# Performance work log

Hardware: AMD Instinct MI355X
Metric: run time of the kernel (lower is better)

Reference implementation:

```python
import jax, jax.numpy as jnp
from jax import lax
import numpy as np

B, EMB, HEADS, LAYERS = 32, 512, 8, 4
SEQ_JD, TOK = 200, 50

def _mask_lg(S):
    # Faithful vectorization of CoKEModel.mask_lg (True = masked)
    m = np.ones((B, HEADS, S, S), dtype=bool)
    rows = np.arange(S)[:, None]
    cols = np.clip(rows - 5 + np.arange(10)[None, :], 0, S - 1)  # window=10, offset -5..4
    for h in range(6):  # local_len = 6 local-window heads
        m[:, h, rows, cols] = False
    m[0, 6:] = False          # global heads unmasked only for batch 0 (faithful to source)
    m[:, :, 0, :] = False     # CLS row attends everywhere
    return m

def _ln_free(x):
    # CoKEModel.layer_norm: no affine, eps=1e-12, rsqrt form
    mu = jnp.mean(x, axis=-1, keepdims=True)
    sx = x - mu
    v = jnp.mean(sx * sx, axis=-1, keepdims=True)
    return sx * jnp.sqrt(1.0 / (v + 1e-12))

def _ln(x, g, b):
    mu = jnp.mean(x, axis=-1, keepdims=True)
    sx = x - mu
    v = jnp.mean(sx * sx, axis=-1, keepdims=True)
    return sx / jnp.sqrt(v + 1e-5) * g + b

def _textcnn(tokens, emb, cws, cbs, fw, fb):
    e = emb[tokens]                        # (N, 50, 1024)
    x = jnp.transpose(e, (0, 2, 1))        # (N, 1024, 50): embed dim as channels
    pooled = []
    for W, b in zip(cws, cbs):             # W: (100, k, 1024)
        rhs = jnp.transpose(W, (0, 2, 1))  # (100, 1024, k)
        y = lax.conv_general_dilated(x, rhs, (1,), 'VALID', dimension_numbers=('NCH', 'OIH', 'NCH'))
        y = jax.nn.relu(y + b[None, :, None])
        pooled.append(jnp.max(y, axis=2))  # global max-pool over time
    return jnp.concatenate(pooled, axis=1) @ fw.T + fb   # (N, 512)

def _encoder(x, mask, wq, bq, wk, bk, wv, bv, wo, bo, l1g, l1b, fw1, fb1, fw2, fb2, l2g, l2b):
    Bb, S, D = x.shape
    dh = D // HEADS
    scale = 1.0 / (dh ** 0.5)
    for l in range(LAYERS):
        q = (x @ wq[l].T + bq[l]).reshape(Bb, S, HEADS, dh)
        k = (x @ wk[l].T + bk[l]).reshape(Bb, S, HEADS, dh)
        v = (x @ wv[l].T + bv[l]).reshape(Bb, S, HEADS, dh)
        s = jnp.einsum('bshd,bthd->bhst', q, k) * scale
        s = jnp.where(mask, -1e9, s)
        a = jax.nn.softmax(s, axis=-1)
        c = jnp.einsum('bhst,bthd->bshd', a, v).reshape(Bb, S, D)
        x = _ln(x + c @ wo[l].T + bo[l], l1g[l], l1b[l])
        h = jax.nn.relu(x @ fw1[l].T + fb1[l])
        x = _ln(x + h @ fw2[l].T + fb2[l], l2g[l], l2b[l])
    return x

def _contrastive(im, s, margin=0.02):
    sc = im @ s.T
    d = jnp.diag(sc)
    cs = jnp.maximum(margin + sc - d[:, None], 0.0)
    ci = jnp.maximum(margin + sc - d[None, :], 0.0)
    eye = jnp.eye(sc.shape[0], dtype=bool)
    cs = jnp.where(eye, 0.0, cs)
    ci = jnp.where(eye, 0.0, ci)
    return jnp.sum(cs) + jnp.sum(ci)

def _forward(floats, src, mask101, mask200):
    (user_info, label_similarity, emb_tc, cw1, cb1, cw2, cb2, cw3, cb3, tfw, tfb,
     wq, bq, wk, bk, wv, bv, wo, bo, l1g, l1b, fw1, fb1, fw2, fb2, l2g, l2b,
     fc1w, fc1b, fc2w, fc2b, fc3w, fc3b, fc4w, fc4b, pscale, pbias) = floats
    cws, cbs = (cw1, cw2, cw3), (cb1, cb2, cb3)
    enc = (wq, bq, wk, bk, wv, bv, wo, bo, l1g, l1b, fw1, fb1, fw2, fb2, l2g, l2b)

    # ---- first pass: first 100 JDs + global CLS token ----
    s1 = _textcnn(src[:, :100].reshape(-1, TOK), emb_tc, cws, cbs, tfw, tfb).reshape(B, 100, EMB)
    s1 = _ln_free(s1)
    s1 = jnp.concatenate([jnp.zeros((B, 1, EMB), s1.dtype), s1], axis=1)  # (B, 101, EMB)
    p = _encoder(s1, mask101, *enc)
    p = jax.nn.gelu(p @ fc1w.T + fc1b, approximate=False)
    p = _ln_free(p)
    p = p * pscale[:, :p.shape[1]] + pbias[:, :p.shape[1]]
    p = p @ fc2w.T + fc2b                      # (B, 101, 204)
    cls_e, tok = p[:, :1], p[:, 1:]
    P = tok @ fc3w.T + fc3b                    # (B, 100, 204)
    clsIII = cls_e @ fc3w.T + fc3b             # (B, 1, 204)
    SLl = jnp.einsum('bsm,bsn->bmn', P, P)     # P^T @ P
    SL_hat = label_similarity[None] + 0.4 * SLl
    outIII = jnp.squeeze(clsIII @ SL_hat, axis=1)  # (B, 204)

    # ---- second pass: all 200 JDs ----
    s2 = _textcnn(src.reshape(-1, TOK), emb_tc, cws, cbs, tfw, tfb).reshape(B, SEQ_JD, EMB)
    s2 = _ln_free(s2)
    ap = _encoder(s2, mask200, *enc)
    ap = jax.nn.gelu(ap @ fc1w.T + fc1b, approximate=False)
    ap = _ln_free(ap)
    ap = ap * pscale[:, :SEQ_JD] + pbias[:, :SEQ_JD]
    p1 = ap @ fc2w.T + fc2b                    # (B, 200, 204)

    nn_ = SEQ_JD // 100  # = 2 neighbors
    eps = 1e-6
    skl_rows, seuc_rows = [], []
    for i in range(nn_):
        # NOTE: faithful to source slicing bug: [i : (i+1)*100]
        c1 = jax.nn.softmax(jnp.mean(p1[:, i:(i + 1) * 100], axis=1), axis=-1)
        a1 = jax.nn.softmax(jnp.mean(ap[:, i:(i + 1) * 100], axis=1), axis=-1)
        rk, re = [], []
        for j in range(nn_):
            c2 = jax.nn.softmax(jnp.mean(p1[:, j:(j + 1) * 100], axis=1), axis=-1)
            a2 = jax.nn.softmax(jnp.mean(ap[:, j:(j + 1) * 100], axis=1), axis=-1)
            rk.append(jnp.sum((c1 + eps) * jnp.log((c1 + eps) / (c2 + eps)), axis=-1))
            re.append(jnp.sqrt(jnp.sum((a1 - a2) ** 2, axis=-1) + 1e-12))
        skl_rows.append(jnp.stack(rk, axis=-1))
        seuc_rows.append(jnp.stack(re, axis=-1))
    skl = jnp.stack(skl_rows, axis=1).reshape(B, -1) * 10.0
    seuc = jnp.stack(seuc_rows, axis=1).reshape(B, -1)
    skl = jax.nn.softmax(skl, axis=-1)
    seuc = jax.nn.softmax(seuc, axis=-1)
    loss_sims = jnp.mean(jnp.sum((skl + eps) * jnp.log((skl + eps) / (seuc + eps)), axis=-1))

    cls4m = jnp.squeeze(cls_e, axis=1)
    user4m = user_info @ fc4w.T + fc4b
    nrm = lambda x: x / jnp.maximum(jnp.linalg.norm(x, axis=1, keepdims=True), 1e-12)
    match = _contrastive(nrm(cls4m), nrm(user4m))

    return (jax.nn.softmax(outIII, axis=-1),
            jax.nn.softmax(cls_e, axis=-1),
            loss_sims * 100000.0,
            match * 0.01)

def setup_inputs():
    key = jax.random.key(0)
    kit = iter(jax.random.split(key, 48))
    def nrm(shape, s=0.02):
        return jax.random.normal(next(kit), shape, jnp.float32) * s
    d = {}
    d['src'] = jax.random.randint(next(kit), (B, SEQ_JD, TOK), 0, 20000)
    d['user_info'] = nrm((B, 142), 1.0)
    d['label_similarity'] = nrm((204, 204))
    d['emb_tc'] = nrm((20000, 1024)).at[0].set(0.0)  # padding_idx=0 row zeroed
    d['cw1'], d['cb1'] = nrm((100, 1, 1024)), jnp.zeros((100,), jnp.float32)
    d['cw2'], d['cb2'] = nrm((100, 2, 1024)), jnp.zeros((100,), jnp.float32)
    d['cw3'], d['cb3'] = nrm((100, 3, 1024)), jnp.zeros((100,), jnp.float32)
    d['tfw'], d['tfb'] = nrm((512, 300)), jnp.zeros((512,), jnp.float32)
    d['wq'], d['bq'] = nrm((LAYERS, EMB, EMB)), jnp.zeros((LAYERS, EMB), jnp.float32)
    d['wk'], d['bk'] = nrm((LAYERS, EMB, EMB)), jnp.zeros((LAYERS, EMB), jnp.float32)
    d['wv'], d['bv'] = nrm((LAYERS, EMB, EMB)), jnp.zeros((LAYERS, EMB), jnp.float32)
    d['wo'], d['bo'] = nrm((LAYERS, EMB, EMB)), jnp.zeros((LAYERS, EMB), jnp.float32)
    d['l1g'], d['l1b'] = jnp.ones((LAYERS, EMB), jnp.float32), jnp.zeros((LAYERS, EMB), jnp.float32)
    d['fw1'], d['fb1'] = nrm((LAYERS, 2048, EMB)), jnp.zeros((LAYERS, 2048), jnp.float32)
    d['fw2'], d['fb2'] = nrm((LAYERS, EMB, 2048)), jnp.zeros((LAYERS, EMB), jnp.float32)
    d['l2g'], d['l2b'] = jnp.ones((LAYERS, EMB), jnp.float32), jnp.zeros((LAYERS, EMB), jnp.float32)
    d['fc1w'], d['fc1b'] = nrm((EMB, EMB)), jnp.zeros((EMB,), jnp.float32)
    d['fc2w'], d['fc2b'] = nrm((204, EMB)), jnp.zeros((204,), jnp.float32)
    d['fc3w'], d['fc3b'] = nrm((204, 204)), jnp.zeros((204,), jnp.float32)
    d['fc4w'], d['fc4b'] = nrm((204, 142)), jnp.zeros((204,), jnp.float32)
    d['pscale'] = jnp.ones((B, 300, EMB), jnp.float32)
    d['pbias'] = jnp.zeros((B, 300, EMB), jnp.float32)
    d['mask101'] = jnp.asarray(_mask_lg(101))
    d['mask200'] = jnp.asarray(_mask_lg(SEQ_JD))
    return d

def reference(src, user_info, label_similarity, emb_tc, cw1, cb1, cw2, cb2, cw3, cb3, tfw, tfb, wq, bq, wk, bk, wv, bv, wo, bo, l1g, l1b, fw1, fb1, fw2, fb2, l2g, l2b, fc1w, fc1b, fc2w, fc2b, fc3w, fc3b, fc4w, fc4b, pscale, pbias, mask101, mask200):
    floats = (user_info, label_similarity, emb_tc, cw1, cb1, cw2, cb2, cw3, cb3, tfw, tfb,
              wq, bq, wk, bk, wv, bv, wo, bo, l1g, l1b, fw1, fb1, fw2, fb2, l2g, l2b,
              fc1w, fc1b, fc2w, fc2b, fc3w, fc3b, fc4w, fc4b, pscale, pbias)
    return _forward(floats, src, mask101, mask200)
```

## Files before the change

kernel.cpp:

```cpp
#include <hip/hip_runtime.h>
#include <math.h>

#define EMB 512
#define HEADS 8
#define NLAYERS 4
#define NB 32
#define SEQ 200
#define TOKN 50
#define DH 64
#define FFND 2048
#define NCLS 204
#define VC 640
#define KD 1024
#define CCH 8
#define CROWS (6400/CCH)
#define CM (CROWS*TOKN)
#define MSEG 16

typedef __attribute__((ext_vector_type(8))) short v8s;
typedef __attribute__((ext_vector_type(4))) float v4f;
typedef unsigned short ushort_t;

__device__ __forceinline__ ushort_t f2bu(float f){
  unsigned u = __float_as_uint(f);
  return (ushort_t)((u + 0x7FFFu + ((u >> 16) & 1u)) >> 16);
}
__device__ __forceinline__ float bu2f(ushort_t u){
  return __uint_as_float(((unsigned)u) << 16);
}

__device__ __forceinline__ float block_reduce(float v, float* red, int nwaves, bool domax){
  int tid = threadIdx.x;
  #pragma unroll
  for (int o = 32; o > 0; o >>= 1){
    float t = __shfl_down(v, o, 64);
    v = domax ? fmaxf(v, t) : (v + t);
  }
  __syncthreads();
  if ((tid & 63) == 0) red[tid >> 6] = v;
  __syncthreads();
  float r = red[0];
  for (int i = 1; i < nwaves; i++) r = domax ? fmaxf(r, red[i]) : (r + red[i]);
  return r;
}

__global__ void prep_w_kernel(const float* __restrict__ cw1, const float* __restrict__ cw2,
                              const float* __restrict__ cw3, ushort_t* __restrict__ Wb){
  int idx4 = blockIdx.x * 256 + threadIdx.x;
  if (idx4 >= VC * KD / 4) return;
  int row = idx4 >> 8;
  int k = (idx4 & 255) * 4;
  float4 v = make_float4(0.f, 0.f, 0.f, 0.f);
  const float* s = nullptr;
  if (row < 100)      s = cw1 + (size_t)row * KD;
  else if (row < 200) s = cw2 + (size_t)((row - 100) * 2 + 0) * KD;
  else if (row < 300) s = cw2 + (size_t)((row - 200) * 2 + 1) * KD;
  else if (row < 400) s = cw3 + (size_t)((row - 300) * 3 + 0) * KD;
  else if (row < 500) s = cw3 + (size_t)((row - 400) * 3 + 1) * KD;
  else if (row < 600) s = cw3 + (size_t)((row - 500) * 3 + 2) * KD;
  if (s) v = *(const float4*)(s + k);
  ushort4 o;
  o.x = f2bu(v.x); o.y = f2bu(v.y); o.z = f2bu(v.z); o.w = f2bu(v.w);
  *(ushort4*)(Wb + (size_t)row * KD + k) = o;
}

__global__ void prep_tfwT_kernel(const float* __restrict__ tfw, float* __restrict__ tfwT){
  int idx = blockIdx.x * 256 + threadIdx.x;
  if (idx >= 300 * EMB) return;
  int j = idx >> 9, o = idx & 511;
  tfwT[(size_t)j * EMB + o] = tfw[(size_t)o * 300 + j];
}

__global__ void split_kernel(const float* __restrict__ src, ushort_t* __restrict__ hi,
                             ushort_t* __restrict__ lo, int n){
  int i4 = (blockIdx.x * 256 + threadIdx.x) * 4;
  if (i4 >= n) return;
  float4 f = *(const float4*)(src + i4);
  float x[4] = {f.x, f.y, f.z, f.w};
  ushort4 h, l;
  ushort_t hh[4], ll[4];
  #pragma unroll
  for (int e = 0; e < 4; e++){
    unsigned u = __float_as_uint(x[e]);
    float hf = __uint_as_float(u & 0xFFFF0000u);
    hh[e] = (ushort_t)(u >> 16);
    ll[e] = f2bu(x[e] - hf);
  }
  h.x=hh[0]; h.y=hh[1]; h.z=hh[2]; h.w=hh[3];
  l.x=ll[0]; l.y=ll[1]; l.z=ll[2]; l.w=ll[3];
  *(ushort4*)(hi + i4) = h;
  *(ushort4*)(lo + i4) = l;
}

__global__ void qkvbias_kernel(const float* __restrict__ bq, const float* __restrict__ bk,
                               const float* __restrict__ bv, float* __restrict__ bqkv){
  int l = blockIdx.x;
  for (int j = threadIdx.x; j < 1536; j += 256){
    float v;
    if (j < 512) v = bq[l * 512 + j];
    else if (j < 1024) v = bk[l * 512 + j - 512];
    else v = bv[l * 512 + j - 1024];
    bqkv[l * 1536 + j] = v;
  }
}

__global__ __launch_bounds__(256, 4) void conv_gemm_kernel(
    const int* __restrict__ tok, const float* __restrict__ emb,
    const ushort_t* __restrict__ Wb, ushort_t* __restrict__ Cout, int Mc)
{
  __shared__ ushort_t Al[128][40];
  __shared__ ushort_t Bl[128][40];
  const int tid = threadIdx.x;
  const int n0 = blockIdx.x * 128;
  const int m0 = blockIdx.y * 128;
  const int wave = tid >> 6, lane = tid & 63;
  const int wm = (wave >> 1) * 64, wn = (wave & 1) * 64;
  const int lcol = lane & 15, lq = lane >> 4;

  v4f acc[4][4];
  #pragma unroll
  for (int i = 0; i < 4; i++)
    #pragma unroll
    for (int j = 0; j < 4; j++) acc[i][j] = (v4f){0.f, 0.f, 0.f, 0.f};

  const int srow = tid >> 1, skh = (tid & 1) * 16;
  const int am = m0 + srow;
  const float* aep = (am < Mc) ? (emb + (size_t)tok[am] * KD + skh) : nullptr;
  const ushort_t* bep = Wb + (size_t)(n0 + srow) * KD + skh;

  for (int k0 = 0; k0 < KD; k0 += 32){
    uint4 p0 = make_uint4(0,0,0,0), p1 = make_uint4(0,0,0,0);
    if (aep){
      float4 f0 = *(const float4*)(aep + k0);
      float4 f1 = *(const float4*)(aep + k0 + 4);
      float4 f2 = *(const float4*)(aep + k0 + 8);
      float4 f3 = *(const float4*)(aep + k0 + 12);
      p0.x = (unsigned)f2bu(f0.x) | ((unsigned)f2bu(f0.y) << 16);
      p0.y = (unsigned)f2bu(f0.z) | ((unsigned)f2bu(f0.w) << 16);
      p0.z = (unsigned)f2bu(f1.x) | ((unsigned)f2bu(f1.y) << 16);
      p0.w = (unsigned)f2bu(f1.z) | ((unsigned)f2bu(f1.w) << 16);
      p1.x = (unsigned)f2bu(f2.x) | ((unsigned)f2bu(f2.y) << 16);
      p1.y = (unsigned)f2bu(f2.z) | ((unsigned)f2bu(f2.w) << 16);
      p1.z = (unsigned)f2bu(f3.x) | ((unsigned)f2bu(f3.y) << 16);
      p1.w = (unsigned)f2bu(f3.z) | ((unsigned)f2bu(f3.w) << 16);
    }
    *(uint4*)&Al[srow][skh]     = p0;
    *(uint4*)&Al[srow][skh + 8] = p1;
    uint4 b0 = *(const uint4*)(bep + k0);
    uint4 b1 = *(const uint4*)(bep + k0 + 8);
    *(uint4*)&Bl[srow][skh]     = b0;
    *(uint4*)&Bl[srow][skh + 8] = b1;
    __syncthreads();

    v8s af[4];
    #pragma unroll
    for (int mi = 0; mi < 4; mi++)
      af[mi] = *(const v8s*)&Al[wm + mi*16 + lcol][lq*8];
    #pragma unroll
    for (int ni = 0; ni < 4; ni++){
      v8s bf = *(const v8s*)&Bl[wn + ni*16 + lcol][lq*8];
      #pragma unroll
      for (int mi = 0; mi < 4; mi++)
        acc[mi][ni] = __builtin_amdgcn_mfma_f32_16x16x32_bf16(af[mi], bf, acc[mi][ni], 0, 0, 0);
    }
    __syncthreads();
  }

  #pragma unroll
  for (int ni = 0; ni < 4; ni++){
    int n = n0 + wn + ni*16 + lcol;
    #pragma unroll
    for (int mi = 0; mi < 4; mi++){
      int mbase = m0 + wm + mi*16 + lq*4;
      #pragma unroll
      for (int rg = 0; rg < 4; rg++){
        int m = mbase + rg;
        if (m < Mc) Cout[(size_t)m * VC + n] = f2bu(acc[mi][ni][rg]);
      }
    }
  }
}

__global__ __launch_bounds__(256, 2) void pool_fc_kernel(
    const ushort_t* __restrict__ Cc, const float* __restrict__ tfwT,
    const float* __restrict__ cb1, const float* __restrict__ cb2,
    const float* __restrict__ cb3, const float* __restrict__ tfb,
    float* __restrict__ basep)
{
  __shared__ ushort_t Sg[VC][54];
  __shared__ float pooled[304];
  __shared__ float red[8];
  const int tid = threadIdx.x;
  const int r = blockIdx.x;

  const unsigned* cr = (const unsigned*)(Cc + (size_t)r * TOKN * VC);
  for (int p = 0; p < TOKN; p++){
    for (int t = tid; t < VC/2; t += 256){
      unsigned u = cr[p * (VC/2) + t];
      Sg[2*t][p]   = (ushort_t)(u & 0xFFFFu);
      Sg[2*t+1][p] = (ushort_t)(u >> 16);
    }
  }
  __syncthreads();

  for (int c = tid; c < 300; c += 256){
    float mv = -1e30f;
    if (c < 100){
      float bb = cb1[c];
      for (int p = 0; p < 50; p++) mv = fmaxf(mv, bu2f(Sg[c][p]) + bb);
    } else if (c < 200){
      int o = c - 100; float bb = cb2[o];
      for (int p = 0; p < 49; p++)
        mv = fmaxf(mv, bu2f(Sg[100 + o][p]) + bu2f(Sg[200 + o][p + 1]) + bb);
    } else {
      int o = c - 200; float bb = cb3[o];
      for (int p = 0; p < 48; p++)
        mv = fmaxf(mv, bu2f(Sg[300 + o][p]) + bu2f(Sg[400 + o][p + 1]) + bu2f(Sg[500 + o][p + 2]) + bb);
    }
    pooled[c] = fmaxf(mv, 0.f);
  }
  __syncthreads();

  float v0 = tfb[tid], v1 = tfb[tid + 256];
  for (int j = 0; j < 300; j++){
    float pj = pooled[j];
    v0 = fmaf(pj, tfwT[(size_t)j * EMB + tid], v0);
    v1 = fmaf(pj, tfwT[(size_t)j * EMB + tid + 256], v1);
  }
  float tot = block_reduce(v0 + v1, red, 4, false);
  float mu = tot * (1.f / 512.f);
  float s0 = v0 - mu, s1 = v1 - mu;
  float var = block_reduce(s0 * s0 + s1 * s1, red, 4, false) * (1.f / 512.f);
  float sc = sqrtf(1.f / (var + 1e-12f));
  basep[(size_t)r * EMB + tid] = s0 * sc;
  basep[(size_t)r * EMB + tid + 256] = s1 * sc;
}

__global__ __launch_bounds__(256, 3) void gemm_mfma_pre_kernel(
    const float* __restrict__ A, const ushort_t* __restrict__ Whi,
    const ushort_t* __restrict__ Wlo, const float* __restrict__ bias,
    float* __restrict__ C, int M, int N, int K, int ldc, int act)
{
  __shared__ ushort_t Ahi[128][40];
  __shared__ ushort_t Alo[128][40];
  __shared__ ushort_t Bhi[128][40];
  __shared__ ushort_t Blo[128][40];

  const int tid = threadIdx.x;
  const int m0 = blockIdx.y * 128, n0 = blockIdx.x * 128;
  const int wave = tid >> 6, lane = tid & 63;
  const int wm = (wave >> 1) * 64, wn = (wave & 1) * 64;
  const int lcol = lane & 15, lq = lane >> 4;

  v4f acc[4][4];
  #pragma unroll
  for (int i = 0; i < 4; i++)
    #pragma unroll
    for (int j = 0; j < 4; j++) acc[i][j] = (v4f){0.f, 0.f, 0.f, 0.f};

  const int srow = tid >> 1;
  const int skh  = (tid & 1) * 16;
  const int am = m0 + srow, bn = n0 + srow;
  const bool mok = (am < M), nok = (bn < N);
  const float* ap = A + (size_t)am * K + skh;
  const ushort_t* bph = Whi + (size_t)bn * K + skh;
  const ushort_t* bpl = Wlo + (size_t)bn * K + skh;

  for (int k0 = 0; k0 < K; k0 += 32){
    bool kfull = (k0 + 32 <= K);
    {
      float av[16];
      if (mok && kfull){
        #pragma unroll
        for (int q = 0; q < 4; q++){
          float4 f = *(const float4*)(ap + k0 + q*4);
          av[q*4+0]=f.x; av[q*4+1]=f.y; av[q*4+2]=f.z; av[q*4+3]=f.w;
        }
      } else {
        #pragma unroll
        for (int e = 0; e < 16; e++){
          int k = k0 + skh + e;
          av[e] = (mok && k < K) ? ap[k0 + e] : 0.f;
        }
      }
      uint4 uh[2], ul[2];
      #pragma unroll
      for (int h = 0; h < 2; h++){
        unsigned hw[8], lw[8];
        #pragma unroll
        for (int e = 0; e < 8; e++){
          float x = av[h*8+e];
          unsigned u = __float_as_uint(x);
          float hf = __uint_as_float(u & 0xFFFF0000u);
          hw[e] = u >> 16;
          lw[e] = f2bu(x - hf);
        }
        uh[h] = make_uint4(hw[0]|(hw[1]<<16), hw[2]|(hw[3]<<16), hw[4]|(hw[5]<<16), hw[6]|(hw[7]<<16));
        ul[h] = make_uint4(lw[0]|(lw[1]<<16), lw[2]|(lw[3]<<16), lw[4]|(lw[5]<<16), lw[6]|(lw[7]<<16));
      }
      *(uint4*)&Ahi[srow][skh]     = uh[0];
      *(uint4*)&Ahi[srow][skh + 8] = uh[1];
      *(uint4*)&Alo[srow][skh]     = ul[0];
      *(uint4*)&Alo[srow][skh + 8] = ul[1];
    }
    {
      uint4 h0 = make_uint4(0,0,0,0), h1 = h0, l0 = h0, l1 = h0;
      if (nok && kfull){
        h0 = *(const uint4*)(bph + k0);
        h1 = *(const uint4*)(bph + k0 + 8);
        l0 = *(const uint4*)(bpl + k0);
        l1 = *(const uint4*)(bpl + k0 + 8);
      } else if (nok){
        ushort_t he[16], le[16];
        #pragma unroll
        for (int e = 0; e < 16; e++){
          int k = k0 + skh + e;
          he[e] = (k < K) ? bph[k0 + e] : (ushort_t)0;
          le[e] = (k < K) ? bpl[k0 + e] : (ushort_t)0;
        }
        h0 = *(uint4*)&he[0]; h1 = *(uint4*)&he[8];
        l0 = *(uint4*)&le[0]; l1 = *(uint4*)&le[8];
      }
      *(uint4*)&Bhi[srow][skh]     = h0;
      *(uint4*)&Bhi[srow][skh + 8] = h1;
      *(uint4*)&Blo[srow][skh]     = l0;
      *(uint4*)&Blo[srow][skh + 8] = l1;
    }
    __syncthreads();

    v8s ah[4], al[4];
    #pragma unroll
    for (int mi = 0; mi < 4; mi++){
      ah[mi] = *(const v8s*)&Ahi[wm + mi*16 + lcol][lq*8];
      al[mi] = *(const v8s*)&Alo[wm + mi*16 + lcol][lq*8];
    }
    #pragma unroll
    for (int ni = 0; ni < 4; ni++){
      v8s bh = *(const v8s*)&Bhi[wn + ni*16 + lcol][lq*8];
      v8s bl = *(const v8s*)&Blo[wn + ni*16 + lcol][lq*8];
      #pragma unroll
      for (int mi = 0; mi < 4; mi++){
        acc[mi][ni] = __builtin_amdgcn_mfma_f32_16x16x32_bf16(ah[mi], bh, acc[mi][ni], 0, 0, 0);
        acc[mi][ni] = __builtin_amdgcn_mfma_f32_16x16x32_bf16(al[mi], bh, acc[mi][ni], 0, 0, 0);
        acc[mi][ni] = __builtin_amdgcn_mfma_f32_16x16x32_bf16(ah[mi], bl, acc[mi][ni], 0, 0, 0);
      }
    }
    __syncthreads();
  }

  #pragma unroll
  for (int ni = 0; ni < 4; ni++){
    int n = n0 + wn + ni*16 + lcol;
    if (n >= N) continue;
    float bv = bias[n];
    #pragma unroll
    for (int mi = 0; mi < 4; mi++){
      int mbase = m0 + wm + mi*16 + lq*4;
      #pragma unroll
      for (int rg = 0; rg < 4; rg++){
        int m = mbase + rg;
        if (m >= M) continue;
        float v = acc[mi][ni][rg] + bv;
        if (act == 1) v = fmaxf(v, 0.f);
        else if (act == 2) v = 0.5f * v * (1.f + erff(v * 0.70710678118654752f));
        C[(size_t)m * ldc + n] = v;
      }
    }
  }
}

__global__ __launch_bounds__(256, 2) void gemm_mfma_kernel(
    const float* __restrict__ A, const float* __restrict__ W,
    const float* __restrict__ bias, float* __restrict__ C,
    int M, int N, int K, int ldc, int act)
{
  __shared__ ushort_t Ahi[128][40];
  __shared__ ushort_t Alo[128][40];
  __shared__ ushort_t Bhi[128][40];
  __shared__ ushort_t Blo[128][40];

  const int tid = threadIdx.x;
  const int m0 = blockIdx.y * 128, n0 = blockIdx.x * 128;
  const int wave = tid >> 6, lane = tid & 63;
  const int wm = (wave >> 1) * 64, wn = (wave & 1) * 64;
  const int lcol = lane & 15, lq = lane >> 4;

  v4f acc[4][4];
  #pragma unroll
  for (int i = 0; i < 4; i++)
    #pragma unroll
    for (int j = 0; j < 4; j++) acc[i][j] = (v4f){0.f, 0.f, 0.f, 0.f};

  const int srow = tid >> 1;
  const int skh  = (tid & 1) * 16;

  for (int k0 = 0; k0 < K; k0 += 32){
    {
      float av[16];
      int m = m0 + srow;
      const float* ap = A + (size_t)m * K + k0 + skh;
      bool mok = (m < M);
      if (mok && (k0 + 32 <= K)){
        #pragma unroll
        for (int q = 0; q < 4; q++){
          float4 f = ((const float4*)ap)[q];
          av[q*4+0]=f.x; av[q*4+1]=f.y; av[q*4+2]=f.z; av[q*4+3]=f.w;
        }
      } else {
        #pragma unroll
        for (int e = 0; e < 16; e++){
          int k = k0 + skh + e;
          av[e] = (mok && k < K) ? ap[e] : 0.f;
        }
      }
      uint4 uh[2], ul[2];
      #pragma unroll
      for (int h = 0; h < 2; h++){
        unsigned hw[8], lw[8];
        #pragma unroll
        for (int e = 0; e < 8; e++){
          float x = av[h*8+e];
          unsigned u = __float_as_uint(x);
          float hf = __uint_as_float(u & 0xFFFF0000u);
          hw[e] = u >> 16;
          lw[e] = f2bu(x - hf);
        }
        uh[h] = make_uint4(hw[0]|(hw[1]<<16), hw[2]|(hw[3]<<16), hw[4]|(hw[5]<<16), hw[6]|(hw[7]<<16));
        ul[h] = make_uint4(lw[0]|(lw[1]<<16), lw[2]|(lw[3]<<16), lw[4]|(lw[5]<<16), lw[6]|(lw[7]<<16));
      }
      *(uint4*)&Ahi[srow][skh]     = uh[0];
      *(uint4*)&Ahi[srow][skh + 8] = uh[1];
      *(uint4*)&Alo[srow][skh]     = ul[0];
      *(uint4*)&Alo[srow][skh + 8] = ul[1];
    }
    {
      float bv[16];
      int n = n0 + srow;
      const float* bp = W + (size_t)n * K + k0 + skh;
      bool nok = (n < N);
      if (nok && (k0 + 32 <= K)){
        #pragma unroll
        for (int q = 0; q < 4; q++){
          float4 f = ((const float4*)bp)[q];
          bv[q*4+0]=f.x; bv[q*4+1]=f.y; bv[q*4+2]=f.z; bv[q*4+3]=f.w;
        }
      } else {
        #pragma unroll
        for (int e = 0; e < 16; e++){
          int k = k0 + skh + e;
          bv[e] = (nok && k < K) ? bp[e] : 0.f;
        }
      }
      uint4 uh[2], ul[2];
      #pragma unroll
      for (int h = 0; h < 2; h++){
        unsigned hw[8], lw[8];
        #pragma unroll
        for (int e = 0; e < 8; e++){
          float x = bv[h*8+e];
          unsigned u = __float_as_uint(x);
          float hf = __uint_as_float(u & 0xFFFF0000u);
          hw[e] = u >> 16;
          lw[e] = f2bu(x - hf);
        }
        uh[h] = make_uint4(hw[0]|(hw[1]<<16), hw[2]|(hw[3]<<16), hw[4]|(hw[5]<<16), hw[6]|(hw[7]<<16));
        ul[h] = make_uint4(lw[0]|(lw[1]<<16), lw[2]|(lw[3]<<16), lw[4]|(lw[5]<<16), lw[6]|(lw[7]<<16));
      }
      *(uint4*)&Bhi[srow][skh]     = uh[0];
      *(uint4*)&Bhi[srow][skh + 8] = uh[1];
      *(uint4*)&Blo[srow][skh]     = ul[0];
      *(uint4*)&Blo[srow][skh + 8] = ul[1];
    }
    __syncthreads();

    v8s ah[4], al[4];
    #pragma unroll
    for (int mi = 0; mi < 4; mi++){
      ah[mi] = *(const v8s*)&Ahi[wm + mi*16 + lcol][lq*8];
      al[mi] = *(const v8s*)&Alo[wm + mi*16 + lcol][lq*8];
    }
    #pragma unroll
    for (int ni = 0; ni < 4; ni++){
      v8s bh = *(const v8s*)&Bhi[wn + ni*16 + lcol][lq*8];
      v8s bl = *(const v8s*)&Blo[wn + ni*16 + lcol][lq*8];
      #pragma unroll
      for (int mi = 0; mi < 4; mi++){
        acc[mi][ni] = __builtin_amdgcn_mfma_f32_16x16x32_bf16(ah[mi], bh, acc[mi][ni], 0, 0, 0);
        acc[mi][ni] = __builtin_amdgcn_mfma_f32_16x16x32_bf16(al[mi], bh, acc[mi][ni], 0, 0, 0);
        acc[mi][ni] = __builtin_amdgcn_mfma_f32_16x16x32_bf16(ah[mi], bl, acc[mi][ni], 0, 0, 0);
      }
    }
    __syncthreads();
  }

  #pragma unroll
  for (int ni = 0; ni < 4; ni++){
    int n = n0 + wn + ni*16 + lcol;
    if (n >= N) continue;
    float bv = bias[n];
    #pragma unroll
    for (int mi = 0; mi < 4; mi++){
      int mbase = m0 + wm + mi*16 + lq*4;
      #pragma unroll
      for (int rg = 0; rg < 4; rg++){
        int m = mbase + rg;
        if (m >= M) continue;
        float v = acc[mi][ni][rg] + bv;
        if (act == 1) v = fmaxf(v, 0.f);
        else if (act == 2) v = 0.5f * v * (1.f + erff(v * 0.70710678118654752f));
        C[(size_t)m * ldc + n] = v;
      }
    }
  }
}

__global__ __launch_bounds__(256) void gemm_kernel(
    const float* __restrict__ A, const float* __restrict__ W,
    const float* __restrict__ bias, float* __restrict__ C,
    int M, int N, int K, int act)
{
  __shared__ float As[16][64];
  __shared__ float Ws[16][64];
  const int tid = threadIdx.x;
  const int m0 = blockIdx.y * 64, n0 = blockIdx.x * 64;
  const int lr = tid >> 2;
  const int lk = (tid & 3) * 4;
  const int tx = tid & 15, ty = tid >> 4;
  float cc[4][4];
  #pragma unroll
  for (int i = 0; i < 4; i++)
    #pragma unroll
    for (int j = 0; j < 4; j++) cc[i][j] = 0.f;

  for (int k0 = 0; k0 < K; k0 += 16){
    #pragma unroll
    for (int i = 0; i < 4; i++){
      int k = k0 + lk + i;
      int m = m0 + lr;
      As[lk + i][lr] = (m < M && k < K) ? A[(size_t)m * K + k] : 0.f;
      int n = n0 + lr;
      Ws[lk + i][lr] = (n < N && k < K) ? W[(size_t)n * K + k] : 0.f;
    }
    __syncthreads();
    #pragma unroll
    for (int kk = 0; kk < 16; kk++){
      float4 a = *(const float4*)&As[kk][ty * 4];
      float4 b = *(const float4*)&Ws[kk][tx * 4];
      float av[4] = {a.x, a.y, a.z, a.w};
      float bv[4] = {b.x, b.y, b.z, b.w};
      #pragma unroll
      for (int i = 0; i < 4; i++)
        #pragma unroll
        for (int j = 0; j < 4; j++) cc[i][j] = fmaf(av[i], bv[j], cc[i][j]);
    }
    __syncthreads();
  }

  #pragma unroll
  for (int i = 0; i < 4; i++){
    int m = m0 + ty * 4 + i;
    if (m >= M) continue;
    #pragma unroll
    for (int j = 0; j < 4; j++){
      int n = n0 + tx * 4 + j;
      if (n >= N) continue;
      float v = cc[i][j] + bias[n];
      if (act == 1) v = fmaxf(v, 0.f);
      else if (act == 2) v = 0.5f * v * (1.f + erff(v * 0.70710678118654752f));
      C[(size_t)m * N + n] = v;
    }
  }
}

__global__ __launch_bounds__(256) void ln_kernel(
    const float* __restrict__ X, const float* __restrict__ Res,
    const float* __restrict__ g, const float* __restrict__ bta,
    const float* __restrict__ pscale, const float* __restrict__ pbias,
    float* __restrict__ Y, int S, float eps)
{
  __shared__ float red[8];
  const int r = blockIdx.x, tid = threadIdx.x;
  size_t o0 = (size_t)r * EMB + tid;
  size_t o1 = o0 + 256;
  float v0 = X[o0] + (Res ? Res[o0] : 0.f);
  float v1 = X[o1] + (Res ? Res[o1] : 0.f);
  float tot = block_reduce(v0 + v1, red, 4, false);
  float mu = tot * (1.f / 512.f);
  float s0 = v0 - mu, s1 = v1 - mu;
  float var = block_reduce(s0 * s0 + s1 * s1, red, 4, false) * (1.f / 512.f);
  float rs = 1.f / sqrtf(var + eps);
  float y0 = s0 * rs, y1 = s1 * rs;
  if (g){
    y0 = y0 * g[tid] + bta[tid];
    y1 = y1 * g[tid + 256] + bta[tid + 256];
  }
  if (pscale){
    int b = r / S, t = r % S;
    size_t po = ((size_t)(b * 300 + t)) * EMB;
    y0 = y0 * pscale[po + tid] + pbias[po + tid];
    y1 = y1 * pscale[po + tid + 256] + pbias[po + tid + 256];
  }
  Y[o0] = y0;
  Y[o1] = y1;
}

__global__ __launch_bounds__(64) void vmean_kernel(const float* __restrict__ qkv,
                                                   float* __restrict__ vm, int S){
  int bh = blockIdx.x; int b = bh >> 3, h = bh & 7; int d = threadIdx.x;
  const float* vr = qkv + (size_t)(b * S) * 1536 + 1024 + h * DH + d;
  float s = 0.f;
  for (int j = 0; j < S; j++) s += vr[(size_t)j * 1536];
  vm[bh * DH + d] = s / (float)S;
}

__global__ __launch_bounds__(64) void attn_kernel(
    const float* __restrict__ qkv, const float* __restrict__ vm,
    float* __restrict__ Ctx, int S)
{
  __shared__ float qv[DH];
  __shared__ float sc[SEQ];
  __shared__ float wts[16];
  const int tid = threadIdx.x;
  const int blk = blockIdx.x;
  const int i = blk % S;
  const int bh = blk / S;
  const int h = bh % HEADS;
  const int b = bh / HEADS;
  const size_t rowoff = ((size_t)(b * S + i)) * 1536 + h * DH;
  const size_t coff = ((size_t)(b * S + i)) * EMB + h * DH;
  const bool rowall = (i == 0) || (b == 0 && h >= 6);

  if (rowall){
    qv[tid] = qkv[rowoff + tid];
    __syncthreads();
    for (int j = tid; j < S; j += 64){
      const float* kr = qkv + ((size_t)(b * S + j)) * 1536 + 512 + h * DH;
      float d = 0.f;
      #pragma unroll
      for (int d4 = 0; d4 < 16; d4++){
        float4 kk = *(const float4*)(kr + d4 * 4);
        d = fmaf(qv[d4*4+0], kk.x, d);
        d = fmaf(qv[d4*4+1], kk.y, d);
        d = fmaf(qv[d4*4+2], kk.z, d);
        d = fmaf(qv[d4*4+3], kk.w, d);
      }
      sc[j] = d * 0.125f;
    }
    __syncthreads();
    float mx = -INFINITY;
    for (int j = tid; j < S; j += 64) mx = fmaxf(mx, sc[j]);
    #pragma unroll
    for (int o = 32; o > 0; o >>= 1) mx = fmaxf(mx, __shfl_down(mx, o, 64));
    mx = __shfl(mx, 0, 64);
    float sm = 0.f;
    for (int j = tid; j < S; j += 64){ float e = expf(sc[j] - mx); sc[j] = e; sm += e; }
    #pragma unroll
    for (int o = 32; o > 0; o >>= 1) sm += __shfl_down(sm, o, 64);
    sm = __shfl(sm, 0, 64);
    float inv = 1.f / sm;
    __syncthreads();
    float a_ = 0.f;
    const float* vr = qkv + ((size_t)(b * S)) * 1536 + 1024 + h * DH + tid;
    for (int j = 0; j < S; j++) a_ = fmaf(sc[j], vr[(size_t)j * 1536], a_);
    Ctx[coff + tid] = a_ * inv;
  } else if (h < 6){
    qv[tid] = qkv[rowoff + tid];
    __syncthreads();
    const int lo = max(0, i - 5), hi = min(S - 1, i + 4);
    const int cnt = hi - lo + 1;
    float s = -INFINITY;
    if (tid < cnt){
      const float* kr = qkv + ((size_t)(b * S + lo + tid)) * 1536 + 512 + h * DH;
      float d = 0.f;
      #pragma unroll
      for (int d4 = 0; d4 < 16; d4++){
        float4 kk = *(const float4*)(kr + d4 * 4);
        d = fmaf(qv[d4*4+0], kk.x, d);
        d = fmaf(qv[d4*4+1], kk.y, d);
        d = fmaf(qv[d4*4+2], kk.z, d);
        d = fmaf(qv[d4*4+3], kk.w, d);
      }
      s = d * 0.125f;
    }
    float mx = s;
    #pragma unroll
    for (int o = 8; o > 0; o >>= 1) mx = fmaxf(mx, __shfl_xor(mx, o, 16));
    float e = (tid < cnt) ? expf(s - mx) : 0.f;
    float sm = e;
    #pragma unroll
    for (int o = 8; o > 0; o >>= 1) sm += __shfl_xor(sm, o, 16);
    if (tid < 16) wts[tid] = e / sm;
    __syncthreads();
    float a_ = 0.f;
    const float* vr = qkv + ((size_t)(b * S + lo)) * 1536 + 1024 + h * DH + tid;
    for (int j = 0; j < cnt; j++) a_ = fmaf(wts[j], vr[(size_t)j * 1536], a_);
    Ctx[coff + tid] = a_;
  } else {
    Ctx[coff + tid] = vm[(b * HEADS + h) * DH + tid];
  }
}

__global__ void buildx1_kernel(const float* __restrict__ base, float* __restrict__ x1){
  int idx = blockIdx.x * 256 + threadIdx.x;
  if (idx >= NB * 101 * EMB) return;
  int e = idx & 511;
  int bt = idx >> 9;
  int t = bt % 101, b = bt / 101;
  x1[idx] = (t == 0) ? 0.f : base[((size_t)(b * SEQ + t - 1)) * EMB + e];
}

__global__ void extract_kernel(const float* __restrict__ p2, float* __restrict__ clsE, float* __restrict__ tok){
  int idx = blockIdx.x * 256 + threadIdx.x;
  if (idx >= NB * 101 * NCLS) return;
  int n = idx % NCLS;
  int bt = idx / NCLS;
  int t = bt % 101, b = bt / 101;
  float v = p2[idx];
  if (t == 0) clsE[b * NCLS + n] = v;
  else tok[((size_t)(b * 100 + t - 1)) * NCLS + n] = v;
}

__global__ void zero_kernel(float* p){ if (threadIdx.x == 0) p[0] = 0.f; }

__global__ __launch_bounds__(256) void slhat_kernel(
    const float* __restrict__ P, const float* __restrict__ ls, float* __restrict__ SLh)
{
  int bm = blockIdx.x;
  int b = bm / NCLS, m = bm % NCLS;
  int n = threadIdx.x;
  if (n >= NCLS) return;
  const float* Pb = P + (size_t)b * 100 * NCLS;
  float s = 0.f;
  for (int t = 0; t < 100; t++) s = fmaf(Pb[t * NCLS + m], Pb[t * NCLS + n], s);
  SLh[((size_t)bm) * NCLS + n] = ls[m * NCLS + n] + 0.4f * s;
}

__global__ __launch_bounds__(256) void outIII_kernel(
    const float* __restrict__ cls3, const float* __restrict__ SLh, float* __restrict__ o3)
{
  int b = blockIdx.x, n = threadIdx.x;
  if (n >= NCLS) return;
  float s = 0.f;
  for (int m = 0; m < NCLS; m++)
    s = fmaf(cls3[b * NCLS + m], SLh[((size_t)(b * NCLS + m)) * NCLS + n], s);
  o3[b * NCLS + n] = s;
}

__global__ __launch_bounds__(256) void softmax_out_kernel(const float* __restrict__ X, float* __restrict__ O, int n){
  __shared__ float red[8];
  int r = blockIdx.x, tid = threadIdx.x;
  float mx = -INFINITY;
  for (int j = tid; j < n; j += 256) mx = fmaxf(mx, X[(size_t)r * n + j]);
  mx = block_reduce(mx, red, 4, true);
  float sm = 0.f;
  for (int j = tid; j < n; j += 256) sm += expf(X[(size_t)r * n + j] - mx);
  sm = block_reduce(sm, red, 4, false);
  for (int j = tid; j < n; j += 256) O[(size_t)r * n + j] = expf(X[(size_t)r * n + j] - mx) / sm;
}

__global__ __launch_bounds__(256) void normalize_kernel(
    const float* __restrict__ clsE, const float* __restrict__ u4,
    float* __restrict__ imn, float* __restrict__ sn)
{
  __shared__ float red[8];
  int r = blockIdx.x, tid = threadIdx.x;
  const float* s = (r < NB) ? (clsE + (size_t)r * NCLS) : (u4 + (size_t)(r - NB) * NCLS);
  float* d = (r < NB) ? (imn + (size_t)r * NCLS) : (sn + (size_t)(r - NB) * NCLS);
  float v = (tid < NCLS) ? s[tid] : 0.f;
  float ss = block_reduce(v * v, red, 4, false);
  float nrm = fmaxf(sqrtf(ss), 1e-12f);
  if (tid < NCLS) d[tid] = v / nrm;
}

__global__ __launch_bounds__(1024) void contrastive_kernel(
    const float* __restrict__ imn, const float* __restrict__ sn, float* __restrict__ out)
{
  __shared__ float sc[NB][NB];
  __shared__ float red[16];
  int tid = threadIdx.x;
  int i = tid >> 5, j = tid & 31;
  float d = 0.f;
  for (int c = 0; c < NCLS; c++) d = fmaf(imn[i * NCLS + c], sn[j * NCLS + c], d);
  sc[i][j] = d;
  __syncthreads();
  float di = sc[i][i], dj = sc[j][j];
  float v = 0.f;
  if (i != j)
    v = fmaxf(0.02f + sc[i][j] - di, 0.f) + fmaxf(0.02f + sc[i][j] - dj, 0.f);
  #pragma unroll
  for (int o = 32; o > 0; o >>= 1) v += __shfl_down(v, o, 64);
  if ((tid & 63) == 0) red[tid >> 6] = v;
  __syncthreads();
  if (tid == 0){
    float s = 0.f;
    for (int w = 0; w < 16; w++) s += red[w];
    out[13057] = s * 0.01f;
  }
}

__global__ __launch_bounds__(256) void means_part_kernel(
    const float* __restrict__ p1, const float* __restrict__ ap,
    float* __restrict__ part)
{
  const int blk = blockIdx.x;
  const int bi = blk / MSEG, seg = blk % MSEG;
  const int b = bi >> 1, i = bi & 1;
  const int start = i;
  const int cnt = (i == 0) ? 100 : 199;
  const int per = (cnt + MSEG - 1) / MSEG;
  const int r0 = seg * per;
  const int r1 = min(r0 + per, cnt);
  float* dst = part + (size_t)blk * 720;
  for (int c = threadIdx.x; c < NCLS + EMB; c += 256){
    float s = 0.f;
    if (c < NCLS){
      for (int rr = r0; rr < r1; rr++)
        s += p1[((size_t)(b * SEQ + start + rr)) * NCLS + c];
    } else {
      int cc = c - NCLS;
      for (int rr = r0; rr < r1; rr++)
        s += ap[((size_t)(b * SEQ + start + rr)) * EMB + cc];
    }
    dst[c] = s;
  }
}

__global__ __launch_bounds__(256) void means_final_kernel(
    const float* __restrict__ part, float* __restrict__ mp, float* __restrict__ ma)
{
  const int bi = blockIdx.x;
  const int i = bi & 1;
  const float icnt = (i == 0) ? (1.f / 100.f) : (1.f / 199.f);
  for (int c = threadIdx.x; c < NCLS + EMB; c += 256){
    float s = 0.f;
    #pragma unroll
    for (int g = 0; g < MSEG; g++)
      s += part[((size_t)(bi * MSEG + g)) * 720 + c];
    if (c < NCLS) mp[(size_t)bi * NCLS + c] = s * icnt;
    else          ma[(size_t)bi * EMB + (c - NCLS)] = s * icnt;
  }
}

__global__ __launch_bounds__(64) void klfinal_kernel(
    const float* __restrict__ cbuf, const float* __restrict__ abuf, float* __restrict__ acc)
{
  const int b = blockIdx.x, lane = threadIdx.x;
  float rk[4], re[4];
  #pragma unroll
  for (int pr = 0; pr < 4; pr++){
    int i = pr >> 1, j = pr & 1;
    const float* c1 = cbuf + ((size_t)(b * 2 + i)) * NCLS;
    const float* c2 = cbuf + ((size_t)(b * 2 + j)) * NCLS;
    float s = 0.f;
    for (int n = lane; n < NCLS; n += 64){
      float x = c1[n] + 1e-6f, y = c2[n] + 1e-6f;
      s += x * logf(x / y);
    }
    #pragma unroll
    for (int o = 32; o > 0; o >>= 1) s += __shfl_down(s, o, 64);
    rk[pr] = __shfl(s, 0, 64);
    const float* a1 = abuf + ((size_t)(b * 2 + i)) * EMB;
    const float* a2 = abuf + ((size_t)(b * 2 + j)) * EMB;
    float s2 = 0.f;
    for (int n = lane; n < EMB; n += 64){
      float dd = a1[n] - a2[n];
      s2 += dd * dd;
    }
    #pragma unroll
    for (int o = 32; o > 0; o >>= 1) s2 += __shfl_down(s2, o, 64);
    re[pr] = sqrtf(__shfl(s2, 0, 64) + 1e-12f);
  }
  if (lane == 0){
    float sk[4], se[4];
    float mk = -INFINITY, me = -INFINITY;
    for (int p = 0; p < 4; p++){
      sk[p] = rk[p] * 10.f;
      mk = fmaxf(mk, sk[p]);
      se[p] = re[p];
      me = fmaxf(me, se[p]);
    }
    float ssk = 0.f, sse = 0.f;
    for (int p = 0; p < 4; p++){ sk[p] = expf(sk[p] - mk); ssk += sk[p]; se[p] = expf(se[p] - me); sse += se[p]; }
    float loss = 0.f;
    for (int p = 0; p < 4; p++){
      float x = sk[p] / ssk + 1e-6f, y = se[p] / sse + 1e-6f;
      loss += x * logf(x / y);
    }
    atomicAdd(acc, loss);
  }
}

__global__ void finalize_kernel(const float* __restrict__ acc, float* __restrict__ out){
  if (threadIdx.x == 0) out[13056] = acc[0] * (100000.f / 32.f);
}

extern "C" void kernel_launch(void* const* d_in, const int* in_sizes, int n_in,
                              void* d_out, int out_size, void* d_ws, size_t ws_size,
                              hipStream_t stream)
{
  (void)in_sizes; (void)n_in; (void)out_size;
  const int*   src  = (const int*)  d_in[0];
  const float* user_info = (const float*)d_in[1];
  const float* ls   = (const float*)d_in[2];
  const float* emb  = (const float*)d_in[3];
  const float* cw1  = (const float*)d_in[4];  const float* cb1 = (const float*)d_in[5];
  const float* cw2  = (const float*)d_in[6];  const float* cb2 = (const float*)d_in[7];
  const float* cw3  = (const float*)d_in[8];  const float* cb3 = (const float*)d_in[9];
  const float* tfw  = (const float*)d_in[10]; const float* tfb = (const float*)d_in[11];
  const float* wq   = (const float*)d_in[12]; const float* bq  = (const float*)d_in[13];
  const float* wk   = (const float*)d_in[14]; const float* bk  = (const float*)d_in[15];
  const float* wv   = (const float*)d_in[16]; const float* bv  = (const float*)d_in[17];
  const float* wo   = (const float*)d_in[18]; const float* bo  = (const float*)d_in[19];
  const float* l1g  = (const float*)d_in[20]; const float* l1b = (const float*)d_in[21];
  const float* fw1  = (const float*)d_in[22]; const float* fb1 = (const float*)d_in[23];
  const float* fw2  = (const float*)d_in[24]; const float* fb2 = (const float*)d_in[25];
  const float* l2g  = (const float*)d_in[26]; const float* l2b = (const float*)d_in[27];
  const float* fc1w = (const float*)d_in[28]; const float* fc1b= (const float*)d_in[29];
  const float* fc2w = (const float*)d_in[30]; const float* fc2b= (const float*)d_in[31];
  const float* fc3w = (const float*)d_in[32]; const float* fc3b= (const float*)d_in[33];
  const float* fc4w = (const float*)d_in[34]; const float* fc4b= (const float*)d_in[35];
  const float* pscale = (const float*)d_in[36];
  const float* pbias  = (const float*)d_in[37];
  float* out = (float*)d_out;
  float* ws = (float*)d_ws;

  size_t off = 0;
  auto alloc = [&](size_t n){ float* p = ws + off; off += ((n + 3) & ~(size_t)3); return p; };
  float* base = alloc(6400ULL * EMB);
  float* x1   = alloc((size_t)NB * 101 * EMB);
  float* qkv  = alloc(6400ULL * 1536);
  float* ctx  = alloc(6400ULL * EMB);
  float* proj = alloc(6400ULL * EMB);
  float* hb   = alloc(6400ULL * FFND);
  float* p2   = alloc(6400ULL * NCLS);
  float* clsE = alloc((size_t)NB * NCLS);
  float* tok  = alloc(3200ULL * NCLS);
  float* Pb   = alloc(3200ULL * NCLS);
  float* cls3 = alloc((size_t)NB * NCLS);
  float* SLh  = alloc((size_t)NB * NCLS * NCLS);
  float* o3   = alloc((size_t)NB * NCLS);
  float* u4   = alloc((size_t)NB * NCLS);
  float* imn  = alloc((size_t)NB * NCLS);
  float* sn   = alloc((size_t)NB * NCLS);
  float* mp   = alloc(64ULL * NCLS);
  float* ma   = alloc(64ULL * EMB);
  float* cbf  = alloc(64ULL * NCLS);
  float* abf  = alloc(64ULL * EMB);
  float* lacc = alloc(4);
  float* vmb  = alloc((size_t)NB * HEADS * DH);
  ushort_t* Wb = (ushort_t*)alloc((size_t)VC * KD / 2);
  float* tfwT = alloc(300ULL * EMB);
  float* bqkv = alloc(4ULL * 1536);
  const size_t OQKV = 0, OWO = 3145728, OF1 = 4194304, OF2 = 8388608;
  const size_t OC1 = 12582912, OC2 = 12845056, OC3 = 12949504, WTOT = 12991120;
  ushort_t* WhiA = (ushort_t*)alloc((WTOT + 1) / 2);
  ushort_t* WloA = (ushort_t*)alloc((WTOT + 1) / 2);
  const bool presplit = (off * sizeof(float) <= ws_size);

  auto gemm_f32 = [&](const float* A, const float* W, const float* bi, float* C,
                      int M, int N, int K, int act){
    dim3 g((N + 63) / 64, (M + 63) / 64);
    gemm_kernel<<<g, 256, 0, stream>>>(A, W, bi, C, M, N, K, act);
  };
  auto gemm_fly = [&](const float* A, const float* W, const float* bi, float* C,
                      int M, int N, int K, int ldc, int act){
    dim3 g((N + 127) / 128, (M + 127) / 128);
    gemm_mfma_kernel<<<g, 256, 0, stream>>>(A, W, bi, C, M, N, K, ldc, act);
  };
  auto gemm_pre = [&](const float* A, size_t woff, const float* bi, float* C,
                      int M, int N, int K, int ldc, int act){
    dim3 g((N + 127) / 128, (M + 127) / 128);
    gemm_mfma_pre_kernel<<<g, 256, 0, stream>>>(A, WhiA + woff, WloA + woff, bi, C, M, N, K, ldc, act);
  };
  auto split = [&](const float* srcw, size_t woff, int n){
    split_kernel<<<(n / 4 + 255) / 256, 256, 0, stream>>>(srcw, WhiA + woff, WloA + woff, n);
  };

  prep_w_kernel<<<(VC * KD / 4 + 255) / 256, 256, 0, stream>>>(cw1, cw2, cw3, Wb);
  prep_tfwT_kernel<<<(300 * EMB + 255) / 256, 256, 0, stream>>>(tfw, tfwT);
  if (presplit){
    for (int l = 0; l < NLAYERS; l++){
      split(wq + (size_t)l * 262144, OQKV + (size_t)l * 786432,          262144);
      split(wk + (size_t)l * 262144, OQKV + (size_t)l * 786432 + 262144, 262144);
      split(wv + (size_t)l * 262144, OQKV + (size_t)l * 786432 + 524288, 262144);
      split(wo + (size_t)l * 262144, OWO + (size_t)l * 262144, 262144);
      split(fw1 + (size_t)l * 1048576, OF1 + (size_t)l * 1048576, 1048576);
      split(fw2 + (size_t)l * 1048576, OF2 + (size_t)l * 1048576, 1048576);
    }
    split(fc1w, OC1, 262144);
    split(fc2w, OC2, NCLS * EMB);
    split(fc3w, OC3, NCLS * NCLS);
    qkvbias_kernel<<<4, 256, 0, stream>>>(bq, bk, bv, bqkv);
  }

  for (int c = 0; c < CCH; c++){
    conv_gemm_kernel<<<dim3(VC / 128, (CM + 127) / 128), 256, 0, stream>>>(
        src + (size_t)c * CM, emb, Wb, (ushort_t*)hb, CM);
    pool_fc_kernel<<<CROWS, 256, 0, stream>>>(
        (ushort_t*)hb, tfwT, cb1, cb2, cb3, tfb, base + (size_t)c * CROWS * EMB);
  }
  buildx1_kernel<<<(NB * 101 * EMB + 255) / 256, 256, 0, stream>>>(base, x1);

  auto encoder = [&](float* x, int S){
    int M = NB * S;
    for (int l = 0; l < NLAYERS; l++){
      if (presplit){
        gemm_pre(x, OQKV + (size_t)l * 786432, bqkv + l * 1536, qkv, M, 1536, EMB, 1536, 0);
      } else {
        gemm_fly(x, wq + (size_t)l * EMB * EMB, bq + l * EMB, qkv,        M, EMB, EMB, 1536, 0);
        gemm_fly(x, wk + (size_t)l * EMB * EMB, bk + l * EMB, qkv + 512,  M, EMB, EMB, 1536, 0);
        gemm_fly(x, wv + (size_t)l * EMB * EMB, bv + l * EMB, qkv + 1024, M, EMB, EMB, 1536, 0);
      }
      vmean_kernel<<<NB * HEADS, 64, 0, stream>>>(qkv, vmb, S);
      attn_kernel<<<NB * HEADS * S, 64, 0, stream>>>(qkv, vmb, ctx, S);
      if (presplit) gemm_pre(ctx, OWO + (size_t)l * 262144, bo + l * EMB, proj, M, EMB, EMB, EMB, 0);
      else gemm_fly(ctx, wo + (size_t)l * EMB * EMB, bo + l * EMB, proj, M, EMB, EMB, EMB, 0);
      ln_kernel<<<M, 256, 0, stream>>>(proj, x, l1g + l * EMB, l1b + l * EMB, nullptr, nullptr, x, S, 1e-5f);
      if (presplit) gemm_pre(x, OF1 + (size_t)l * 1048576, fb1 + l * FFND, hb, M, FFND, EMB, FFND, 1);
      else gemm_fly(x, fw1 + (size_t)l * FFND * EMB, fb1 + l * FFND, hb, M, FFND, EMB, FFND, 1);
      if (presplit) gemm_pre(hb, OF2 + (size_t)l * 1048576, fb2 + l * EMB, proj, M, EMB, FFND, EMB, 0);
      else gemm_fly(hb, fw2 + (size_t)l * EMB * FFND, fb2 + l * EMB, proj, M, EMB, FFND, EMB, 0);
      ln_kernel<<<M, 256, 0, stream>>>(proj, x, l2g + l * EMB, l2b + l * EMB, nullptr, nullptr, x, S, 1e-5f);
    }
    if (presplit) gemm_pre(x, OC1, fc1b, ctx, M, EMB, EMB, EMB, 2);
    else gemm_fly(x, fc1w, fc1b, ctx, M, EMB, EMB, EMB, 2);
    ln_kernel<<<M, 256, 0, stream>>>(ctx, nullptr, nullptr, nullptr, pscale, pbias, ctx, S, 1e-12f);
    if (presplit) gemm_pre(ctx, OC2, fc2b, p2, M, NCLS, EMB, NCLS, 0);
    else gemm_fly(ctx, fc2w, fc2b, p2, M, NCLS, EMB, NCLS, 0);
  };

  encoder(x1, 101);
  extract_kernel<<<(NB * 101 * NCLS + 255) / 256, 256, 0, stream>>>(p2, clsE, tok);
  if (presplit) gemm_pre(tok, OC3, fc3b, Pb, 3200, NCLS, NCLS, NCLS, 0);
  else gemm_fly(tok, fc3w, fc3b, Pb, 3200, NCLS, NCLS, NCLS, 0);
  gemm_f32(clsE, fc3w, fc3b, cls3, NB, NCLS, NCLS, 0);
  slhat_kernel<<<NB * NCLS, 256, 0, stream>>>(Pb, ls, SLh);
  outIII_kernel<<<NB, 256, 0, stream>>>(cls3, SLh, o3);
  softmax_out_kernel<<<NB, 256, 0, stream>>>(o3, out, NCLS);
  softmax_out_kernel<<<NB, 256, 0, stream>>>(clsE, out + NB * NCLS, NCLS);
  gemm_f32(user_info, fc4w, fc4b, u4, NB, NCLS, 142, 0);
  normalize_kernel<<<64, 256, 0, stream>>>(clsE, u4, imn, sn);
  contrastive_kernel<<<1, 1024, 0, stream>>>(imn, sn, out);

  encoder(base, SEQ);
  zero_kernel<<<1, 64, 0, stream>>>(lacc);
  means_part_kernel<<<64 * MSEG, 256, 0, stream>>>(p2, ctx, hb);
  means_final_kernel<<<64, 256, 0, stream>>>(hb, mp, ma);
  softmax_out_kernel<<<64, 256, 0, stream>>>(mp, cbf, NCLS);
  softmax_out_kernel<<<64, 256, 0, stream>>>(ma, abf, EMB);
  klfinal_kernel<<<NB, 64, 0, stream>>>(cbf, abf, lacc);
  finalize_kernel<<<1, 64, 0, stream>>>(lacc, out);
}
```

Measured before the change: 5.916 ms.

## Pre-convert embedding table to bf16 and remap conv GEMM tiles per XCD

Adds a one-time pass that converts the fp32 embedding table to bf16, stored in the qkv scratch buffer. The conv GEMM then gathers bf16 rows directly, which halves the gather bytes and removes the per-tile conversion work. The conv GEMM grid is also flattened to 1D, with a remap that gives each of the 8 XCDs a contiguous range of tiles to improve L2 locality. The trade-off is an extra conversion pass over the full 20000x1024 table, and reusing qkv as storage assumes nothing else needs that buffer before the encoder runs.

```diff
diff --git a/kernel.cpp b/kernel.cpp
--- a/kernel.cpp
+++ b/kernel.cpp
@@ -16,6 +16,9 @@
 #define CROWS (6400/CCH)
 #define CM (CROWS*TOKN)
 #define MSEG 16
+#define CMT ((CM + 127) / 128)
+#define CNT (VC / 128)
+#define CT  (CMT * CNT)
 
 typedef __attribute__((ext_vector_type(8))) short v8s;
 typedef __attribute__((ext_vector_type(4))) float v4f;
@@ -64,6 +67,15 @@
   *(ushort4*)(Wb + (size_t)row * KD + k) = o;
 }
 
+__global__ void prep_embbf_kernel(const float* __restrict__ emb, ushort_t* __restrict__ embb){
+  size_t i4 = ((size_t)blockIdx.x * 256 + threadIdx.x) * 4;
+  if (i4 >= 20000ULL * KD) return;
+  float4 f = *(const float4*)(emb + i4);
+  ushort4 o;
+  o.x = f2bu(f.x); o.y = f2bu(f.y); o.z = f2bu(f.z); o.w = f2bu(f.w);
+  *(ushort4*)(embb + i4) = o;
+}
+
 __global__ void prep_tfwT_kernel(const float* __restrict__ tfw, float* __restrict__ tfwT){
   int idx = blockIdx.x * 256 + threadIdx.x;
   if (idx >= 300 * EMB) return;
@@ -105,14 +117,18 @@
 }
 
 __global__ __launch_bounds__(256, 4) void conv_gemm_kernel(
-    const int* __restrict__ tok, const float* __restrict__ emb,
+    const int* __restrict__ tok, const ushort_t* __restrict__ embb,
     const ushort_t* __restrict__ Wb, ushort_t* __restrict__ Cout, int Mc)
 {
   __shared__ ushort_t Al[128][40];
   __shared__ ushort_t Bl[128][40];
   const int tid = threadIdx.x;
-  const int n0 = blockIdx.x * 128;
-  const int m0 = blockIdx.y * 128;
+  const int lin = blockIdx.x;
+  const int xcd = lin & 7, idx = lin >> 3;
+  const int q = CT >> 3, r = CT & 7;
+  const int t = ((xcd < r) ? xcd * (q + 1) : r * (q + 1) + (xcd - r) * q) + idx;
+  const int n0 = (t % CNT) * 128;
+  const int m0 = (t / CNT) * 128;
   const int wave = tid >> 6, lane = tid & 63;
   const int wm = (wave >> 1) * 64, wn = (wave & 1) * 64;
   const int lcol = lane & 15, lq = lane >> 4;
@@ -125,27 +141,17 @@
 
   const int srow = tid >> 1, skh = (tid & 1) * 16;
   const int am = m0 + srow;
-  const float* aep = (am < Mc) ? (emb + (size_t)tok[am] * KD + skh) : nullptr;
+  const ushort_t* aep = (am < Mc) ? (embb + (size_t)tok[am] * KD + skh) : nullptr;
   const ushort_t* bep = Wb + (size_t)(n0 + srow) * KD + skh;
 
   for (int k0 = 0; k0 < KD; k0 += 32){
-    uint4 p0 = make_uint4(0,0,0,0), p1 = make_uint4(0,0,0,0);
+    uint4 a0 = make_uint4(0,0,0,0), a1 = make_uint4(0,0,0,0);
     if (aep){
-      float4 f0 = *(const float4*)(aep + k0);
-      float4 f1 = *(const float4*)(aep + k0 + 4);
-      float4 f2 = *(const float4*)(aep + k0 + 8);
-      float4 f3 = *(const float4*)(aep + k0 + 12);
-      p0.x = (unsigned)f2bu(f0.x) | ((unsigned)f2bu(f0.y) << 16);
-      p0.y = (unsigned)f2bu(f0.z) | ((unsigned)f2bu(f0.w) << 16);
-      p0.z = (unsigned)f2bu(f1.x) | ((unsigned)f2bu(f1.y) << 16);
-      p0.w = (unsigned)f2bu(f1.z) | ((unsigned)f2bu(f1.w) << 16);
-      p1.x = (unsigned)f2bu(f2.x) | ((unsigned)f2bu(f2.y) << 16);
-      p1.y = (unsigned)f2bu(f2.z) | ((unsigned)f2bu(f2.w) << 16);
-      p1.z = (unsigned)f2bu(f3.x) | ((unsigned)f2bu(f3.y) << 16);
-      p1.w = (unsigned)f2bu(f3.z) | ((unsigned)f2bu(f3.w) << 16);
-    }
-    *(uint4*)&Al[srow][skh]     = p0;
-    *(uint4*)&Al[srow][skh + 8] = p1;
+      a0 = *(const uint4*)(aep + k0);
+      a1 = *(const uint4*)(aep + k0 + 8);
+    }
+    *(uint4*)&Al[srow][skh]     = a0;
+    *(uint4*)&Al[srow][skh + 8] = a1;
     uint4 b0 = *(const uint4*)(bep + k0);
     uint4 b1 = *(const uint4*)(bep + k0 + 8);
     *(uint4*)&Bl[srow][skh]     = b0;
@@ -951,6 +957,7 @@
   ushort_t* Wb = (ushort_t*)alloc((size_t)VC * KD / 2);
   float* tfwT = alloc(300ULL * EMB);
   float* bqkv = alloc(4ULL * 1536);
+  ushort_t* embb = (ushort_t*)qkv;
   const size_t OQKV = 0, OWO = 3145728, OF1 = 4194304, OF2 = 8388608;
   const size_t OC1 = 12582912, OC2 = 12845056, OC3 = 12949504, WTOT = 12991120;
   ushort_t* WhiA = (ushort_t*)alloc((WTOT + 1) / 2);
@@ -977,6 +984,7 @@
   };
 
   prep_w_kernel<<<(VC * KD / 4 + 255) / 256, 256, 0, stream>>>(cw1, cw2, cw3, Wb);
+  prep_embbf_kernel<<<(int)((20000ULL * KD / 4 + 255) / 256), 256, 0, stream>>>(emb, embb);
   prep_tfwT_kernel<<<(300 * EMB + 255) / 256, 256, 0, stream>>>(tfw, tfwT);
   if (presplit){
     for (int l = 0; l < NLAYERS; l++){
@@ -994,8 +1002,8 @@
   }
 
   for (int c = 0; c < CCH; c++){
-    conv_gemm_kernel<<<dim3(VC / 128, (CM + 127) / 128), 256, 0, stream>>>(
-        src + (size_t)c * CM, emb, Wb, (ushort_t*)hb, CM);
+    conv_gemm_kernel<<<CT, 256, 0, stream>>>(
+        src + (size_t)c * CM, embb, Wb, (ushort_t*)hb, CM);
     pool_fc_kernel<<<CROWS, 256, 0, stream>>>(
         (ushort_t*)hb, tfwT, cb1, cb2, cb3, tfb, base + (size_t)c * CROWS * EMB);
   }
```

Measured after the change: 5.564 ms. 5.9% less time.
